# Performance work log

Measured on AMD Instinct MI355X. Metric: run time of the kernel, lower is better.

## Reference

```python
import jax, jax.numpy as jnp
import numpy as np

N_NODES = 50000
N_EDGES = 400000
N_GRAPHS = 128
IN_DIM = 768
HID = 128
N_CLASSES = 11
BN_EPS = 1e-5


def _sage_conv(x, src, dst, Wl, bl, Wr):
    # PyG SAGEConv (aggr='mean'): out = lin_l(mean_{j->i} x_j) + lin_r(x_i)
    # messages flow src -> dst; nodes with no in-edges get a zero aggregate.
    n = x.shape[0]
    deg = jax.ops.segment_sum(jnp.ones_like(dst, x.dtype), dst, num_segments=n)
    agg = jax.ops.segment_sum(x[src], dst, num_segments=n)  # [N, d] gather+scatter
    agg = agg / jnp.maximum(deg, 1.0)[:, None]
    return agg @ Wl.T + bl + x @ Wr.T


def _batch_norm(x, gamma, beta):
    # training-mode BatchNorm1d: biased batch statistics over the node axis
    m = jnp.mean(x, axis=0)
    v = jnp.var(x, axis=0)
    return (x - m) * jax.lax.rsqrt(v + BN_EPS) * gamma + beta


def setup_inputs() -> dict:
    key = jax.random.key(0)
    ks = jax.random.split(key, 16)
    x = jax.random.normal(ks[0], (N_NODES, IN_DIM), dtype=jnp.float32)
    edge_index = jax.random.randint(ks[1], (2, N_EDGES), 0, N_NODES, dtype=jnp.int32)
    batch = jnp.sort(jax.random.randint(ks[2], (N_NODES,), 0, N_GRAPHS, dtype=jnp.int32))

    def lin_w(k, out_d, in_d):
        return jax.random.normal(k, (out_d, in_d), dtype=jnp.float32) * (1.0 / np.sqrt(in_d))

    params = {
        'W1l': lin_w(ks[3], HID, IN_DIM), 'b1': jnp.zeros((HID,), jnp.float32),
        'W1r': lin_w(ks[4], HID, IN_DIM),
        'g1': jnp.ones((HID,), jnp.float32), 'be1': jnp.zeros((HID,), jnp.float32),
        'W2l': lin_w(ks[5], HID, HID), 'b2': jnp.zeros((HID,), jnp.float32),
        'W2r': lin_w(ks[6], HID, HID),
        'g2': jnp.ones((HID,), jnp.float32), 'be2': jnp.zeros((HID,), jnp.float32),
        'W3l': lin_w(ks[7], HID, HID), 'b3': jnp.zeros((HID,), jnp.float32),
        'W3r': lin_w(ks[8], HID, HID),
        'g3': jnp.ones((HID,), jnp.float32), 'be3': jnp.zeros((HID,), jnp.float32),
        'Wlin': lin_w(ks[9], N_CLASSES, HID), 'blin': jnp.zeros((N_CLASSES,), jnp.float32),
    }
    return {'x': x, 'edge_index': edge_index, 'batch': batch, **params}


def reference(x, edge_index, batch,
              W1l, b1, W1r, g1, be1,
              W2l, b2, W2r, g2, be2,
              W3l, b3, W3r, g3, be3,
              Wlin, blin):
    src, dst = edge_index[0], edge_index[1]
    h = jax.nn.relu(_batch_norm(_sage_conv(x, src, dst, W1l, b1, W1r), g1, be1))
    h = jax.nn.relu(_batch_norm(_sage_conv(h, src, dst, W2l, b2, W2r), g2, be2))
    h = _batch_norm(_sage_conv(h, src, dst, W3l, b3, W3r), g3, be3)
    # global_max_pool over graph ids
    pooled = jax.ops.segment_max(h, batch, num_segments=N_GRAPHS)  # [G, HID]
    # dropout is identity at inference
    return pooled @ Wlin.T + blin  # [G, 11]
```

## Files before the change

### kernel.cpp

```cpp
#include <hip/hip_runtime.h>

#define N_NODESC 50000
#define N_EDGESC 400000
#define N_GRAPHSC 128
#define IN_DIMC 768
#define HIDC 128
#define NCLSC 11
#define BN_EPSC 1e-5f
#define NB_AGG 8
#define NREP 64
#define SCAN_NB ((N_NODESC + 255) / 256)

typedef __bf16 bf16_t;
typedef __bf16 bf16x2 __attribute__((ext_vector_type(2)));
typedef __bf16 bf16x8 __attribute__((ext_vector_type(8)));
typedef float f32x4 __attribute__((ext_vector_type(4)));

typedef __attribute__((address_space(1))) void glb_void;
typedef __attribute__((address_space(3))) void lds_void;

__device__ __forceinline__ void cp16(const void* g, void* l) {
    __builtin_amdgcn_global_load_lds((glb_void*)g, (lds_void*)l, 16, 0, 0);
}

__device__ __forceinline__ f32x4 mfma_16x16x32_bf16(bf16x8 a, bf16x8 b, f32x4 c) {
    return __builtin_amdgcn_mfma_f32_16x16x32_bf16(a, b, c, 0, 0, 0);
}

__global__ __launch_bounds__(256, 2) void gemm_l1_kernel(const float* __restrict__ Av,
                                                         const bf16_t* __restrict__ Wb,
                                                         bf16_t* __restrict__ Cl,
                                                         bf16_t* __restrict__ Cr,
                                                         int M)
{
    constexpr int KC  = IN_DIMC;
    constexpr int NK  = KC / 32;
    constexpr int ASZ = 16384;
    constexpr int BSZ = 16384;
    __shared__ __align__(16) unsigned char smem[2 * ASZ + 2 * BSZ];
    unsigned char* Asm = smem;
    unsigned char* Bsm = smem + 2 * ASZ;

    const int m0   = blockIdx.x * 128;
    const int t    = threadIdx.x;
    const int wid  = t >> 6;
    const int lane = t & 63;
    const int wm   = (wid >> 1) * 64;
    const int l16  = lane & 15;
    const int quad = lane >> 4;

    const char* aSrc[4]; int aDst[4];
#pragma unroll
    for (int s = 0; s < 4; s++) {
        int L = (s * 4 + wid) * 64 + lane;
        int r = L >> 3;
        int c = (L & 7) ^ (r & 7);
        int row = m0 + r; if (row > M - 1) row = M - 1;
        aSrc[s] = (const char*)Av + ((size_t)row * KC + (size_t)c * 4) * 4;
        aDst[s] = (s * 4 + wid) * 1024;
    }
    const char* bSrc[4]; int bDst[4];
#pragma unroll
    for (int s = 0; s < 4; s++) {
        int L = (s * 4 + wid) * 64 + lane;
        int r = L >> 2;
        int c = (L & 3) ^ ((r >> 1) & 3);
        bSrc[s] = (const char*)(Wb + (size_t)r * KC + c * 8);
        bDst[s] = (s * 4 + wid) * 1024;
    }

    int aOff[4][2], bOff[8];
#pragma unroll
    for (int i = 0; i < 4; i++) {
        int ra = wm + i * 16 + l16;
        aOff[i][0] = ra * 128 + (((2 * quad)     ^ (ra & 7)) * 16);
        aOff[i][1] = ra * 128 + (((2 * quad + 1) ^ (ra & 7)) * 16);
    }
    const int wnb = (wid & 1) * 128;
#pragma unroll
    for (int j = 0; j < 8; j++) {
        int rb = wnb + j * 16 + l16;
        bOff[j] = rb * 64 + ((quad ^ ((rb >> 1) & 3)) * 16);
    }

    f32x4 acc[4][8] = {};

#pragma unroll
    for (int s = 0; s < 4; s++) cp16(aSrc[s], Asm + aDst[s]);
#pragma unroll
    for (int s = 0; s < 4; s++) cp16(bSrc[s], Bsm + bDst[s]);

    for (int it = 0; it < NK; ++it) {
        if (it + 1 < NK) {
            const size_t ka = (size_t)(it + 1) * 128;
            const size_t kb = (size_t)(it + 1) * 64;
            const int nb = (it + 1) & 1;
#pragma unroll
            for (int s = 0; s < 4; s++) cp16(aSrc[s] + ka, Asm + nb * ASZ + aDst[s]);
#pragma unroll
            for (int s = 0; s < 4; s++) cp16(bSrc[s] + kb, Bsm + nb * BSZ + bDst[s]);
            asm volatile("s_waitcnt vmcnt(8)" ::: "memory");
        } else {
            asm volatile("s_waitcnt vmcnt(0)" ::: "memory");
        }
        asm volatile("s_barrier" ::: "memory");

        const unsigned char* Ab = Asm + (it & 1) * ASZ;
        const unsigned char* Bb = Bsm + (it & 1) * BSZ;
        bf16x8 af[4], bfr[8];
#pragma unroll
        for (int i = 0; i < 4; i++) {
            float4 u0 = *(const float4*)(Ab + aOff[i][0]);
            float4 u1 = *(const float4*)(Ab + aOff[i][1]);
            af[i][0] = (bf16_t)u0.x; af[i][1] = (bf16_t)u0.y;
            af[i][2] = (bf16_t)u0.z; af[i][3] = (bf16_t)u0.w;
            af[i][4] = (bf16_t)u1.x; af[i][5] = (bf16_t)u1.y;
            af[i][6] = (bf16_t)u1.z; af[i][7] = (bf16_t)u1.w;
        }
#pragma unroll
        for (int j = 0; j < 8; j++)
            bfr[j] = *(const bf16x8*)(Bb + bOff[j]);
#pragma unroll
        for (int i = 0; i < 4; i++)
#pragma unroll
            for (int j = 0; j < 8; j++)
                acc[i][j] = mfma_16x16x32_bf16(af[i], bfr[j], acc[i][j]);

        asm volatile("s_barrier" ::: "memory");
    }

    bf16_t* C = (wid & 1) ? Cr : Cl;
#pragma unroll
    for (int i = 0; i < 4; i++) {
        int rowb = m0 + wm + i * 16 + quad * 4;
#pragma unroll
        for (int j = 0; j < 8; j++) {
            int colh = j * 16 + l16;
#pragma unroll
            for (int rr = 0; rr < 4; rr++) {
                int row = rowb + rr;
                if (row < M) C[(size_t)row * HIDC + colh] = (bf16_t)acc[i][j][rr];
            }
        }
    }
}

__global__ __launch_bounds__(256) void gemm_hid_kernel(const bf16_t* __restrict__ Av,
                                                       const bf16_t* __restrict__ Wb,
                                                       const float* __restrict__ stats,
                                                       const float* __restrict__ g,
                                                       const float* __restrict__ be,
                                                       bf16_t* __restrict__ Cl,
                                                       bf16_t* __restrict__ Cr,
                                                       int M)
{
    constexpr int KC  = HIDC;
    constexpr int NK  = KC / 32;
    constexpr int ASZ = 8192;
    constexpr int BSZ = 8192;
    __shared__ __align__(16) unsigned char smem[3 * ASZ + 3 * BSZ + 1024];
    unsigned char* Asm = smem;
    unsigned char* Bsm = smem + 3 * ASZ;
    float* scS = (float*)(smem + 3 * ASZ + 3 * BSZ);

    const int bid  = blockIdx.x;
    const int p    = ((bid >> 4) << 3) + (bid & 7);
    const int half = (bid >> 3) & 1;
    if (p * 128 >= M) return;
    const int m0 = p * 128;

    const int t    = threadIdx.x;
    const int wid  = t >> 6;
    const int lane = t & 63;
    const int wm   = (wid >> 1) * 64;
    const int wn   = (wid & 1) * 64;
    const int l16  = lane & 15;
    const int quad = lane >> 4;

    const char* bSrc[2]; int bDst[2];
#pragma unroll
    for (int s = 0; s < 2; s++) {
        int L = (s * 4 + wid) * 64 + lane;
        int r = L >> 2;
        int c = (L & 3) ^ ((r >> 1) & 3);
        bSrc[s] = (const char*)(Wb + (size_t)(half * 128 + r) * KC + c * 8);
        bDst[s] = (s * 4 + wid) * 1024;
    }
    const char* aSrc[2]; int aDst[2];
#pragma unroll
    for (int s = 0; s < 2; s++) {
        int L = (s * 4 + wid) * 64 + lane;
        int r = L >> 2;
        int c = (L & 3) ^ ((r >> 1) & 3);
        int row = m0 + r; if (row > M - 1) row = M - 1;
        aSrc[s] = (const char*)Av + ((size_t)row * KC + (size_t)c * 8) * 2;
        aDst[s] = (s * 4 + wid) * 1024;
    }

    int aOff[4], bOff[4];
#pragma unroll
    for (int i = 0; i < 4; i++) {
        int ra = wm + i * 16 + l16;
        aOff[i] = ra * 64 + ((quad ^ ((ra >> 1) & 3)) * 16);
        int rb = wn + i * 16 + l16;
        bOff[i] = rb * 64 + ((quad ^ ((rb >> 1) & 3)) * 16);
    }

    if (t < HIDC) {
        float sum = 0.f, sumsq = 0.f;
        for (int r = 0; r < NREP; r++) {
            sum   += stats[r * 256 + t];
            sumsq += stats[r * 256 + HIDC + t];
        }
        float invM = 1.0f / (float)M;
        float mean = sum * invM;
        float var  = sumsq * invM - mean * mean;
        float s = rsqrtf(var + BN_EPSC) * g[t];
        scS[t] = s;
        scS[HIDC + t] = be[t] - mean * s;
    }
    __syncthreads();

    f32x4 acc[4][4] = {};

#pragma unroll
    for (int s = 0; s < 2; s++) cp16(aSrc[s], Asm + aDst[s]);
#pragma unroll
    for (int s = 0; s < 2; s++) cp16(bSrc[s], Bsm + bDst[s]);
#pragma unroll
    for (int s = 0; s < 2; s++) cp16(aSrc[s] + 64, Asm + ASZ + aDst[s]);
#pragma unroll
    for (int s = 0; s < 2; s++) cp16(bSrc[s] + 64, Bsm + BSZ + bDst[s]);

    for (int it = 0; it < NK; ++it) {
        if (it + 2 < NK) {
            const size_t kb2 = (size_t)(it + 2) * 64;
            const int nb = (it + 2) % 3;
#pragma unroll
            for (int s = 0; s < 2; s++) cp16(aSrc[s] + kb2, Asm + nb * ASZ + aDst[s]);
#pragma unroll
            for (int s = 0; s < 2; s++) cp16(bSrc[s] + kb2, Bsm + nb * BSZ + bDst[s]);
            asm volatile("s_waitcnt vmcnt(8)" ::: "memory");
        } else if (it + 1 < NK) {
            asm volatile("s_waitcnt vmcnt(4)" ::: "memory");
        } else {
            asm volatile("s_waitcnt vmcnt(0)" ::: "memory");
        }
        asm volatile("s_barrier" ::: "memory");

        const unsigned char* Ab = Asm + (it % 3) * ASZ;
        const unsigned char* Bb = Bsm + (it % 3) * BSZ;
        bf16x8 af[4], bfr[4];
        float4 s0 = *(const float4*)&scS[it * 32 + quad * 8];
        float4 s1 = *(const float4*)&scS[it * 32 + quad * 8 + 4];
        float4 h0 = *(const float4*)&scS[HIDC + it * 32 + quad * 8];
        float4 h1 = *(const float4*)&scS[HIDC + it * 32 + quad * 8 + 4];
        float ss[8] = {s0.x, s0.y, s0.z, s0.w, s1.x, s1.y, s1.z, s1.w};
        float hh[8] = {h0.x, h0.y, h0.z, h0.w, h1.x, h1.y, h1.z, h1.w};
#pragma unroll
        for (int i = 0; i < 4; i++) {
            bf16x8 raw = *(const bf16x8*)(Ab + aOff[i]);
#pragma unroll
            for (int e = 0; e < 8; e++)
                af[i][e] = (bf16_t)fmaxf(fmaf((float)raw[e], ss[e], hh[e]), 0.0f);
        }
#pragma unroll
        for (int j = 0; j < 4; j++)
            bfr[j] = *(const bf16x8*)(Bb + bOff[j]);
#pragma unroll
        for (int i = 0; i < 4; i++)
#pragma unroll
            for (int j = 0; j < 4; j++)
                acc[i][j] = mfma_16x16x32_bf16(af[i], bfr[j], acc[i][j]);

        asm volatile("s_barrier" ::: "memory");
    }

    bf16_t* C = half ? Cr : Cl;
#pragma unroll
    for (int i = 0; i < 4; i++) {
        int rowb = m0 + wm + i * 16 + quad * 4;
#pragma unroll
        for (int j = 0; j < 4; j++) {
            int colh = wn + j * 16 + l16;
#pragma unroll
            for (int rr = 0; rr < 4; rr++) {
                int row = rowb + rr;
                if (row < M) C[(size_t)row * HIDC + colh] = (bf16_t)acc[i][j][rr];
            }
        }
    }
}

__global__ void init_kernel(const float* __restrict__ W1l, const float* __restrict__ W1r,
                            const float* __restrict__ W2l, const float* __restrict__ W2r,
                            const float* __restrict__ W3l, const float* __restrict__ W3r,
                            bf16_t* __restrict__ Wb1, bf16_t* __restrict__ Wb2,
                            bf16_t* __restrict__ Wb3,
                            int* __restrict__ degi, float* __restrict__ stats)
{
    const int NW1 = 128 * IN_DIMC;
    const int NW2 = 128 * HIDC;
    const int NS  = 3 * NREP * 256;
    int j = blockIdx.x * blockDim.x + threadIdx.x;
    if (j < 2 * NW1) { Wb1[j] = (bf16_t)((j < NW1) ? W1l[j] : W1r[j - NW1]); return; }
    j -= 2 * NW1;
    if (j < 2 * NW2) { Wb2[j] = (bf16_t)((j < NW2) ? W2l[j] : W2r[j - NW2]); return; }
    j -= 2 * NW2;
    if (j < 2 * NW2) { Wb3[j] = (bf16_t)((j < NW2) ? W3l[j] : W3r[j - NW2]); return; }
    j -= 2 * NW2;
    if (j < NS) { stats[j] = 0.0f; return; }
    j -= NS;
    if (j < N_NODESC) degi[j] = 0;
}

__global__ void degi_kernel(const int* __restrict__ ei, int* __restrict__ degi) {
    int e = blockIdx.x * blockDim.x + threadIdx.x;
    if (e < N_EDGESC) atomicAdd(&degi[ei[N_EDGESC + e]], 1);
}

__global__ __launch_bounds__(256) void scan1_kernel(const int* __restrict__ degi,
                                                    int* __restrict__ local,
                                                    int* __restrict__ partials)
{
    __shared__ int tmp[256];
    const int t = threadIdx.x;
    const int i = blockIdx.x * 256 + t;
    int v = (i < N_NODESC) ? degi[i] : 0;
    tmp[t] = v;
    __syncthreads();
    for (int off = 1; off < 256; off <<= 1) {
        int u = (t >= off) ? tmp[t - off] : 0;
        __syncthreads();
        tmp[t] += u;
        __syncthreads();
    }
    if (i < N_NODESC) local[i] = tmp[t] - v;
    if (t == 255) partials[blockIdx.x] = tmp[255];
}

__global__ __launch_bounds__(256) void scan3_kernel(const int* __restrict__ local,
                                                    const int* __restrict__ partials,
                                                    int* __restrict__ rowptr,
                                                    int* __restrict__ cursor)
{
    __shared__ int inc[256];
    __shared__ int orig[256];
    const int t = threadIdx.x;
    int v = (t < SCAN_NB) ? partials[t] : 0;
    inc[t] = v; orig[t] = v;
    __syncthreads();
    for (int off = 1; off < 256; off <<= 1) {
        int u = (t >= off) ? inc[t - off] : 0;
        __syncthreads();
        inc[t] += u;
        __syncthreads();
    }
    const int boff = inc[blockIdx.x] - orig[blockIdx.x];
    const int i = blockIdx.x * 256 + t;
    if (i < N_NODESC) {
        int r = local[i] + boff;
        rowptr[i] = r;
        cursor[i] = r;
    }
    if (i == 0) rowptr[N_NODESC] = N_EDGESC;
}

__global__ void fill_kernel(const int* __restrict__ ei, int* __restrict__ cursor,
                            int* __restrict__ col) {
    int e = blockIdx.x * blockDim.x + threadIdx.x;
    if (e >= N_EDGESC) return;
    int d = ei[N_EDGESC + e];
    int pos = atomicAdd(&cursor[d], 1);
    col[pos] = ei[e];
}

__global__ __launch_bounds__(128) void agg_combine_kernel(const int* __restrict__ rowptr,
                                                          const int* __restrict__ col,
                                                          const bf16_t* __restrict__ Plb,
                                                          const bf16_t* __restrict__ Prb,
                                                          const float* __restrict__ bias,
                                                          bf16_t* __restrict__ Hb,
                                                          float* __restrict__ stats, int M)
{
    const int lane = threadIdx.x & 63;
    const int wv   = threadIdx.x >> 6;
    const int c0   = lane * 2;
    const float b0 = bias[c0], b1v = bias[c0 + 1];
    const int n0 = blockIdx.x * NB_AGG + wv * (NB_AGG / 2);

    int lo[4], hi[4], pos[4];
    bf16x2 pr[4];
#pragma unroll
    for (int r = 0; r < 4; r++) {
        int n = n0 + r;
        lo[r] = (n < M) ? rowptr[n] : 0;
        hi[r] = (n < M) ? rowptr[n + 1] : 0;
        pos[r] = lo[r];
        if (n < M) pr[r] = *(const bf16x2*)&Prb[(size_t)n * HIDC + c0];
        else { pr[r][0] = (bf16_t)0.f; pr[r][1] = (bf16_t)0.f; }
    }

    float a0[4] = {0.f, 0.f, 0.f, 0.f}, a1[4] = {0.f, 0.f, 0.f, 0.f};

    for (;;) {
        int cnt[4];
        bool any = false;
#pragma unroll
        for (int r = 0; r < 4; r++) {
            int c = hi[r] - pos[r];
            cnt[r] = (c > 8) ? 8 : c;
            if (cnt[r] > 0) any = true;
        }
        if (!any) break;

        bf16x2 v[4][8];
#pragma unroll
        for (int r = 0; r < 4; r++) {
            if (cnt[r] > 0) {
                int idx[8];
#pragma unroll
                for (int j = 0; j < 8; j++) {
                    int ee = pos[r] + j;
                    if (ee > hi[r] - 1) ee = hi[r] - 1;
                    idx[j] = col[ee];
                }
#pragma unroll
                for (int j = 0; j < 8; j++)
                    v[r][j] = *(const bf16x2*)&Plb[(size_t)idx[j] * HIDC + c0];
            }
        }
#pragma unroll
        for (int r = 0; r < 4; r++) {
            if (cnt[r] > 0) {
#pragma unroll
                for (int j = 0; j < 8; j++)
                    if (j < cnt[r]) { a0[r] += (float)v[r][j][0]; a1[r] += (float)v[r][j][1]; }
                pos[r] += cnt[r];
            }
        }
    }

    float s0 = 0.f, s1 = 0.f, q0 = 0.f, q1 = 0.f;
#pragma unroll
    for (int r = 0; r < 4; r++) {
        int n = n0 + r;
        if (n < M) {
            int d = hi[r] - lo[r];
            float inv = 1.0f / (float)(d > 0 ? d : 1);
            float pre0 = fmaf(a0[r], inv, b0) + (float)pr[r][0];
            float pre1 = fmaf(a1[r], inv, b1v) + (float)pr[r][1];
            bf16x2 hv; hv[0] = (bf16_t)pre0; hv[1] = (bf16_t)pre1;
            *(bf16x2*)&Hb[(size_t)n * HIDC + c0] = hv;
            s0 += pre0; s1 += pre1; q0 += pre0 * pre0; q1 += pre1 * pre1;
        }
    }
    const int rep = (blockIdx.x * 2 + wv) & (NREP - 1);
    atomicAdd(&stats[rep * 256 + c0], s0);
    atomicAdd(&stats[rep * 256 + c0 + 1], s1);
    atomicAdd(&stats[rep * 256 + HIDC + c0], q0);
    atomicAdd(&stats[rep * 256 + HIDC + c0 + 1], q1);
}

__global__ __launch_bounds__(128) void poolhead_kernel(const bf16_t* __restrict__ Hb,
                                                       const float* __restrict__ stats,
                                                       const float* __restrict__ g,
                                                       const float* __restrict__ be,
                                                       const int* __restrict__ batch,
                                                       const float* __restrict__ Wlin,
                                                       const float* __restrict__ blin,
                                                       float* __restrict__ out, int M)
{
    __shared__ float sp[HIDC];
    int gph = blockIdx.x;
    int c   = threadIdx.x;
    float sum = 0.f, sumsq = 0.f;
    for (int r = 0; r < NREP; r++) {
        sum   += stats[r * 256 + c];
        sumsq += stats[r * 256 + HIDC + c];
    }
    float invM = 1.0f / (float)M;
    float mean = sum * invM;
    float var  = sumsq * invM - mean * mean;
    float s = rsqrtf(var + BN_EPSC) * g[c];
    float h = be[c] - mean * s;

    int lo = 0, hi = M;
    while (lo < hi) { int m = (lo + hi) >> 1; if (batch[m] < gph) lo = m + 1; else hi = m; }
    int lo2 = lo, hi2 = M;
    while (lo2 < hi2) { int m = (lo2 + hi2) >> 1; if (batch[m] < gph + 1) lo2 = m + 1; else hi2 = m; }
    float mx = -INFINITY;
    for (int rr = lo; rr < lo2; rr++)
        mx = fmaxf(mx, fmaf((float)Hb[(size_t)rr * HIDC + c], s, h));
    sp[c] = mx;
    __syncthreads();
    if (c < NCLSC) {
        float acc = blin[c];
        for (int k = 0; k < HIDC; k++) acc += sp[k] * Wlin[c * HIDC + k];
        out[gph * NCLSC + c] = acc;
    }
}

extern "C" void kernel_launch(void* const* d_in, const int* in_sizes, int n_in,
                              void* d_out, int out_size, void* d_ws, size_t ws_size,
                              hipStream_t stream)
{
    const float* x     = (const float*)d_in[0];
    const int*   ei    = (const int*)d_in[1];
    const int*   batch = (const int*)d_in[2];
    const float* W1l = (const float*)d_in[3];
    const float* b1  = (const float*)d_in[4];
    const float* W1r = (const float*)d_in[5];
    const float* g1  = (const float*)d_in[6];
    const float* be1 = (const float*)d_in[7];
    const float* W2l = (const float*)d_in[8];
    const float* b2  = (const float*)d_in[9];
    const float* W2r = (const float*)d_in[10];
    const float* g2  = (const float*)d_in[11];
    const float* be2 = (const float*)d_in[12];
    const float* W3l = (const float*)d_in[13];
    const float* b3  = (const float*)d_in[14];
    const float* W3r = (const float*)d_in[15];
    const float* g3  = (const float*)d_in[16];
    const float* be3 = (const float*)d_in[17];
    const float* Wlin = (const float*)d_in[18];
    const float* blin = (const float*)d_in[19];

    const int M = N_NODESC;

    char* w = (char*)d_ws;
    bf16_t* Plb  = (bf16_t*)w;  w += (size_t)M * HIDC * 2;
    bf16_t* Prb  = (bf16_t*)w;  w += (size_t)M * HIDC * 2;
    bf16_t* Hb   = (bf16_t*)w;  w += (size_t)M * HIDC * 2;
    bf16_t* Wb1  = (bf16_t*)w;  w += (size_t)256 * IN_DIMC * 2;
    bf16_t* Wb2  = (bf16_t*)w;  w += (size_t)256 * HIDC * 2;
    bf16_t* Wb3  = (bf16_t*)w;  w += (size_t)256 * HIDC * 2;
    int*   rowptr= (int*)w;     w += (size_t)(M + 16) * 4;
    int*   col   = (int*)w;     w += (size_t)N_EDGESC * 4;
    int*   cursor= (int*)w;     w += (size_t)M * 4;
    int*   degi  = (int*)w;     w += (size_t)M * 4;
    int*   slocal= (int*)w;     w += (size_t)M * 4;
    int*   spart = (int*)w;     w += 256 * 4;
    float* stats = (float*)w;   w += (size_t)3 * NREP * 256 * 4;

    float* stats1 = stats;
    float* stats2 = stats + NREP * 256;
    float* stats3 = stats + 2 * NREP * 256;

    const int nP = (M + 127) / 128;
    const dim3 l1_grid(nP);
    const dim3 hid_grid(((nP + 7) / 8) * 16);
    const int agg_blocks = (M + NB_AGG - 1) / NB_AGG;
    const int init_total = 2 * 128 * IN_DIMC + 4 * 128 * HIDC + 3 * NREP * 256 + M;

    init_kernel<<<(init_total + 255) / 256, 256, 0, stream>>>(W1l, W1r, W2l, W2r, W3l, W3r,
                                                              Wb1, Wb2, Wb3, degi, stats);
    degi_kernel<<<(N_EDGESC + 255) / 256, 256, 0, stream>>>(ei, degi);
    scan1_kernel<<<SCAN_NB, 256, 0, stream>>>(degi, slocal, spart);
    scan3_kernel<<<SCAN_NB, 256, 0, stream>>>(slocal, spart, rowptr, cursor);
    fill_kernel<<<(N_EDGESC + 255) / 256, 256, 0, stream>>>(ei, cursor, col);

    gemm_l1_kernel<<<l1_grid, 256, 0, stream>>>(x, Wb1, Plb, Prb, M);
    agg_combine_kernel<<<agg_blocks, 128, 0, stream>>>(rowptr, col, Plb, Prb, b1, Hb, stats1, M);

    gemm_hid_kernel<<<hid_grid, 256, 0, stream>>>(Hb, Wb2, stats1, g1, be1, Plb, Prb, M);
    agg_combine_kernel<<<agg_blocks, 128, 0, stream>>>(rowptr, col, Plb, Prb, b2, Hb, stats2, M);

    gemm_hid_kernel<<<hid_grid, 256, 0, stream>>>(Hb, Wb3, stats2, g2, be2, Plb, Prb, M);
    agg_combine_kernel<<<agg_blocks, 128, 0, stream>>>(rowptr, col, Plb, Prb, b3, Hb, stats3, M);

    poolhead_kernel<<<N_GRAPHSC, 128, 0, stream>>>(Hb, stats3, g3, be3, batch, Wlin, blin,
                                                   (float*)d_out, M);
}
```

Before: 556.8 us.

## Enlarge GEMM tiles to reuse weights across more rows in both GEMM kernels

```diff
diff --git a/kernel.cpp b/kernel.cpp
--- a/kernel.cpp
+++ b/kernel.cpp
@@ -27,7 +27,7 @@
     return __builtin_amdgcn_mfma_f32_16x16x32_bf16(a, b, c, 0, 0, 0);
 }
 
-__global__ __launch_bounds__(256, 2) void gemm_l1_kernel(const float* __restrict__ Av,
+__global__ __launch_bounds__(512, 2) void gemm_l1_kernel(const float* __restrict__ Av,
                                                          const bf16_t* __restrict__ Wb,
                                                          bf16_t* __restrict__ Cl,
                                                          bf16_t* __restrict__ Cr,
@@ -35,38 +35,39 @@
 {
     constexpr int KC  = IN_DIMC;
     constexpr int NK  = KC / 32;
-    constexpr int ASZ = 16384;
+    constexpr int ASZ = 32768;
     constexpr int BSZ = 16384;
     __shared__ __align__(16) unsigned char smem[2 * ASZ + 2 * BSZ];
     unsigned char* Asm = smem;
     unsigned char* Bsm = smem + 2 * ASZ;
 
-    const int m0   = blockIdx.x * 128;
+    const int m0   = blockIdx.x * 256;
     const int t    = threadIdx.x;
     const int wid  = t >> 6;
     const int lane = t & 63;
-    const int wm   = (wid >> 1) * 64;
+    const int wm   = (wid & 3) * 64;
+    const int wnb  = (wid >> 2) * 128;
     const int l16  = lane & 15;
     const int quad = lane >> 4;
 
     const char* aSrc[4]; int aDst[4];
 #pragma unroll
     for (int s = 0; s < 4; s++) {
-        int L = (s * 4 + wid) * 64 + lane;
+        int L = (s * 8 + wid) * 64 + lane;
         int r = L >> 3;
         int c = (L & 7) ^ (r & 7);
         int row = m0 + r; if (row > M - 1) row = M - 1;
         aSrc[s] = (const char*)Av + ((size_t)row * KC + (size_t)c * 4) * 4;
-        aDst[s] = (s * 4 + wid) * 1024;
-    }
-    const char* bSrc[4]; int bDst[4];
-#pragma unroll
-    for (int s = 0; s < 4; s++) {
-        int L = (s * 4 + wid) * 64 + lane;
+        aDst[s] = (s * 8 + wid) * 1024;
+    }
+    const char* bSrc[2]; int bDst[2];
+#pragma unroll
+    for (int s = 0; s < 2; s++) {
+        int L = (s * 8 + wid) * 64 + lane;
         int r = L >> 2;
         int c = (L & 3) ^ ((r >> 1) & 3);
         bSrc[s] = (const char*)(Wb + (size_t)r * KC + c * 8);
-        bDst[s] = (s * 4 + wid) * 1024;
+        bDst[s] = (s * 8 + wid) * 1024;
     }
 
     int aOff[4][2], bOff[8];
@@ -76,7 +77,6 @@
         aOff[i][0] = ra * 128 + (((2 * quad)     ^ (ra & 7)) * 16);
         aOff[i][1] = ra * 128 + (((2 * quad + 1) ^ (ra & 7)) * 16);
     }
-    const int wnb = (wid & 1) * 128;
 #pragma unroll
     for (int j = 0; j < 8; j++) {
         int rb = wnb + j * 16 + l16;
@@ -88,7 +88,7 @@
 #pragma unroll
     for (int s = 0; s < 4; s++) cp16(aSrc[s], Asm + aDst[s]);
 #pragma unroll
-    for (int s = 0; s < 4; s++) cp16(bSrc[s], Bsm + bDst[s]);
+    for (int s = 0; s < 2; s++) cp16(bSrc[s], Bsm + bDst[s]);
 
     for (int it = 0; it < NK; ++it) {
         if (it + 1 < NK) {
@@ -98,8 +98,8 @@
 #pragma unroll
             for (int s = 0; s < 4; s++) cp16(aSrc[s] + ka, Asm + nb * ASZ + aDst[s]);
 #pragma unroll
-            for (int s = 0; s < 4; s++) cp16(bSrc[s] + kb, Bsm + nb * BSZ + bDst[s]);
-            asm volatile("s_waitcnt vmcnt(8)" ::: "memory");
+            for (int s = 0; s < 2; s++) cp16(bSrc[s] + kb, Bsm + nb * BSZ + bDst[s]);
+            asm volatile("s_waitcnt vmcnt(6)" ::: "memory");
         } else {
             asm volatile("s_waitcnt vmcnt(0)" ::: "memory");
         }
@@ -129,7 +129,7 @@
         asm volatile("s_barrier" ::: "memory");
     }
 
-    bf16_t* C = (wid & 1) ? Cr : Cl;
+    bf16_t* C = (wid >> 2) ? Cr : Cl;
 #pragma unroll
     for (int i = 0; i < 4; i++) {
         int rowb = m0 + wm + i * 16 + quad * 4;
@@ -157,35 +157,21 @@
     constexpr int KC  = HIDC;
     constexpr int NK  = KC / 32;
     constexpr int ASZ = 8192;
-    constexpr int BSZ = 8192;
-    __shared__ __align__(16) unsigned char smem[3 * ASZ + 3 * BSZ + 1024];
+    constexpr int BSZ = 16384;
+    __shared__ __align__(16) unsigned char smem[2 * ASZ + 2 * BSZ + 1024];
     unsigned char* Asm = smem;
-    unsigned char* Bsm = smem + 3 * ASZ;
-    float* scS = (float*)(smem + 3 * ASZ + 3 * BSZ);
-
-    const int bid  = blockIdx.x;
-    const int p    = ((bid >> 4) << 3) + (bid & 7);
-    const int half = (bid >> 3) & 1;
-    if (p * 128 >= M) return;
-    const int m0 = p * 128;
-
+    unsigned char* Bsm = smem + 2 * ASZ;
+    float* scS = (float*)(smem + 2 * ASZ + 2 * BSZ);
+
+    const int m0   = blockIdx.x * 128;
     const int t    = threadIdx.x;
     const int wid  = t >> 6;
     const int lane = t & 63;
     const int wm   = (wid >> 1) * 64;
-    const int wn   = (wid & 1) * 64;
+    const int wnb  = (wid & 1) * 128;
     const int l16  = lane & 15;
     const int quad = lane >> 4;
 
-    const char* bSrc[2]; int bDst[2];
-#pragma unroll
-    for (int s = 0; s < 2; s++) {
-        int L = (s * 4 + wid) * 64 + lane;
-        int r = L >> 2;
-        int c = (L & 3) ^ ((r >> 1) & 3);
-        bSrc[s] = (const char*)(Wb + (size_t)(half * 128 + r) * KC + c * 8);
-        bDst[s] = (s * 4 + wid) * 1024;
-    }
     const char* aSrc[2]; int aDst[2];
 #pragma unroll
     for (int s = 0; s < 2; s++) {
@@ -196,14 +182,26 @@
         aSrc[s] = (const char*)Av + ((size_t)row * KC + (size_t)c * 8) * 2;
         aDst[s] = (s * 4 + wid) * 1024;
     }
-
-    int aOff[4], bOff[4];
+    const char* bSrc[4]; int bDst[4];
+#pragma unroll
+    for (int s = 0; s < 4; s++) {
+        int L = (s * 4 + wid) * 64 + lane;
+        int r = L >> 2;
+        int c = (L & 3) ^ ((r >> 1) & 3);
+        bSrc[s] = (const char*)(Wb + (size_t)r * KC + c * 8);
+        bDst[s] = (s * 4 + wid) * 1024;
+    }
+
+    int aOff[4], bOff[8];
 #pragma unroll
     for (int i = 0; i < 4; i++) {
         int ra = wm + i * 16 + l16;
         aOff[i] = ra * 64 + ((quad ^ ((ra >> 1) & 3)) * 16);
-        int rb = wn + i * 16 + l16;
-        bOff[i] = rb * 64 + ((quad ^ ((rb >> 1) & 3)) * 16);
+    }
+#pragma unroll
+    for (int j = 0; j < 8; j++) {
+        int rb = wnb + j * 16 + l16;
+        bOff[j] = rb * 64 + ((quad ^ ((rb >> 1) & 3)) * 16);
     }
 
     if (t < HIDC) {
@@ -221,36 +219,30 @@
     }
     __syncthreads();
 
-    f32x4 acc[4][4] = {};
+    f32x4 acc[4][8] = {};
 
 #pragma unroll
     for (int s = 0; s < 2; s++) cp16(aSrc[s], Asm + aDst[s]);
 #pragma unroll
-    for (int s = 0; s < 2; s++) cp16(bSrc[s], Bsm + bDst[s]);
-#pragma unroll
-    for (int s = 0; s < 2; s++) cp16(aSrc[s] + 64, Asm + ASZ + aDst[s]);
-#pragma unroll
-    for (int s = 0; s < 2; s++) cp16(bSrc[s] + 64, Bsm + BSZ + bDst[s]);
+    for (int s = 0; s < 4; s++) cp16(bSrc[s], Bsm + bDst[s]);
 
     for (int it = 0; it < NK; ++it) {
-        if (it + 2 < NK) {
-            const size_t kb2 = (size_t)(it + 2) * 64;
-            const int nb = (it + 2) % 3;
-#pragma unroll
-            for (int s = 0; s < 2; s++) cp16(aSrc[s] + kb2, Asm + nb * ASZ + aDst[s]);
-#pragma unroll
-            for (int s = 0; s < 2; s++) cp16(bSrc[s] + kb2, Bsm + nb * BSZ + bDst[s]);
-            asm volatile("s_waitcnt vmcnt(8)" ::: "memory");
-        } else if (it + 1 < NK) {
-            asm volatile("s_waitcnt vmcnt(4)" ::: "memory");
+        if (it + 1 < NK) {
+            const size_t ka = (size_t)(it + 1) * 64;
+            const int nb = (it + 1) & 1;
+#pragma unroll
+            for (int s = 0; s < 2; s++) cp16(aSrc[s] + ka, Asm + nb * ASZ + aDst[s]);
+#pragma unroll
+            for (int s = 0; s < 4; s++) cp16(bSrc[s] + ka, Bsm + nb * BSZ + bDst[s]);
+            asm volatile("s_waitcnt vmcnt(6)" ::: "memory");
         } else {
             asm volatile("s_waitcnt vmcnt(0)" ::: "memory");
         }
         asm volatile("s_barrier" ::: "memory");
 
-        const unsigned char* Ab = Asm + (it % 3) * ASZ;
-        const unsigned char* Bb = Bsm + (it % 3) * BSZ;
-        bf16x8 af[4], bfr[4];
+        const unsigned char* Ab = Asm + (it & 1) * ASZ;
+        const unsigned char* Bb = Bsm + (it & 1) * BSZ;
+        bf16x8 af[4], bfr[8];
         float4 s0 = *(const float4*)&scS[it * 32 + quad * 8];
         float4 s1 = *(const float4*)&scS[it * 32 + quad * 8 + 4];
         float4 h0 = *(const float4*)&scS[HIDC + it * 32 + quad * 8];
@@ -265,24 +257,24 @@
                 af[i][e] = (bf16_t)fmaxf(fmaf((float)raw[e], ss[e], hh[e]), 0.0f);
         }
 #pragma unroll
-        for (int j = 0; j < 4; j++)
+        for (int j = 0; j < 8; j++)
             bfr[j] = *(const bf16x8*)(Bb + bOff[j]);
 #pragma unroll
         for (int i = 0; i < 4; i++)
 #pragma unroll
-            for (int j = 0; j < 4; j++)
+            for (int j = 0; j < 8; j++)
                 acc[i][j] = mfma_16x16x32_bf16(af[i], bfr[j], acc[i][j]);
 
         asm volatile("s_barrier" ::: "memory");
     }
 
-    bf16_t* C = half ? Cr : Cl;
+    bf16_t* C = (wid & 1) ? Cr : Cl;
 #pragma unroll
     for (int i = 0; i < 4; i++) {
         int rowb = m0 + wm + i * 16 + quad * 4;
 #pragma unroll
-        for (int j = 0; j < 4; j++) {
-            int colh = wn + j * 16 + l16;
+        for (int j = 0; j < 8; j++) {
+            int colh = j * 16 + l16;
 #pragma unroll
             for (int rr = 0; rr < 4; rr++) {
                 int row = rowb + rr;
@@ -547,9 +539,10 @@
     float* stats2 = stats + NREP * 256;
     float* stats3 = stats + 2 * NREP * 256;
 
-    const int nP = (M + 127) / 128;
-    const dim3 l1_grid(nP);
-    const dim3 hid_grid(((nP + 7) / 8) * 16);
+    const int nP256 = (M + 255) / 256;
+    const int nP128 = (M + 127) / 128;
+    const dim3 l1_grid(nP256);
+    const dim3 hid_grid(nP128);
     const int agg_blocks = (M + NB_AGG - 1) / NB_AGG;
     const int init_total = 2 * 128 * IN_DIMC + 4 * 128 * HIDC + 3 * NREP * 256 + M;
 
@@ -560,7 +553,7 @@
     scan3_kernel<<<SCAN_NB, 256, 0, stream>>>(slocal, spart, rowptr, cursor);
     fill_kernel<<<(N_EDGESC + 255) / 256, 256, 0, stream>>>(ei, cursor, col);
 
-    gemm_l1_kernel<<<l1_grid, 256, 0, stream>>>(x, Wb1, Plb, Prb, M);
+    gemm_l1_kernel<<<l1_grid, 512, 0, stream>>>(x, Wb1, Plb, Prb, M);
     agg_combine_kernel<<<agg_blocks, 128, 0, stream>>>(rowptr, col, Plb, Prb, b1, Hb, stats1, M);
 
     gemm_hid_kernel<<<hid_grid, 256, 0, stream>>>(Hb, Wb2, stats1, g1, be1, Plb, Prb, M);
```

Result: slower. 568.1 us (+2.0%).
